# Kernel tuning notes

Hardware: AMD Instinct MI355X
Metric: run time of the kernel (lower is better)

The kernel has to match this reference:

```python
import jax, jax.numpy as jnp
import numpy as np

K = 2  # diffusion order
N, S, D, L, C = 4000, 32, 128, 2, 10
THETA = 0.5


def setup_inputs() -> dict:
    key = jax.random.key(0)
    ks = jax.random.split(key, 16)
    w = 0.05  # weight scale to keep tanh/exp in sane range
    return {
        "A": jax.random.uniform(ks[0], (N, N), dtype=jnp.float32),
        "embs": jax.random.normal(ks[1], (L, S, N, D), dtype=jnp.float32),
        "conv1_w": jax.random.normal(ks[2], (K, D, D), dtype=jnp.float32) * w,
        "conv2_w": jax.random.normal(ks[3], (K, D, D), dtype=jnp.float32) * w,
        "lin_in_w": jax.random.normal(ks[4], (D, D), dtype=jnp.float32) * w,
        "lin_out_w": jax.random.normal(ks[5], (D, 2 * D), dtype=jnp.float32) * w,
        "W_psi": jax.random.normal(ks[6], (2 * D, D), dtype=jnp.float32) * w,
        "b_psi": jax.random.normal(ks[7], (D,), dtype=jnp.float32) * w,
        "ae": jax.random.uniform(ks[8], (N, 1, 1), dtype=jnp.float32),
        "ab": jax.random.uniform(ks[9], (N, 1, 1), dtype=jnp.float32),
        "emb_table": jax.random.uniform(ks[10], (N, D), minval=-0.1, maxval=0.1, dtype=jnp.float32),
        "W_p": jax.random.normal(ks[11], (D, C), dtype=jnp.float32) * w,
        "W_c": jax.random.normal(ks[12], (D, D), dtype=jnp.float32) * w,
    }


def _diffusion(A_tilde, X, W):
    # A_tilde: [N,N] (sym-normalized); X: [N,S,D] (linear in X, so batching over S
    # is identical to the per-timestep loop); W: [K,D,D]
    P_f = A_tilde / A_tilde.sum(axis=1, keepdims=True)
    P_v = A_tilde.T / A_tilde.sum(axis=0, keepdims=True)
    Z = jnp.einsum('mn,nsd->msd', P_f, X) @ W[0]
    P_psi_f, P_psi_v = P_f, P_v
    for k in range(1, K):
        if k < K // 2:
            P_psi_f = P_psi_f @ P_f
            M = P_psi_f
        else:
            P_psi_v = P_psi_v @ P_v
            M = P_psi_v
        Z = Z + jnp.einsum('mn,nsd->msd', M, X) @ W[k]
    return Z


def _attention(context, lin_in_w, lin_out_w, ae, ab):
    # context: [N,S,D]; query is the last timestep, output_len == 1
    q = context[:, -1, :] @ lin_in_w.T                    # [N,D]
    scores = jnp.einsum('nd,nsd->ns', q, context)         # [N,S]
    attw = jax.nn.softmax(scores, axis=-1)                # [N,S]
    mix = attw[:, None, :] * context.transpose(0, 2, 1)   # [N,D,S]
    delta_t = jnp.arange(S - 1, -1, -1, dtype=context.dtype)  # flipped arange
    bt = jnp.exp(-ab * delta_t[None, None, :])            # [N,1,S]
    term2 = jax.nn.relu(ae * mix * bt)                    # [N,D,S]
    mix_sum = (term2 + mix).sum(axis=-1)                  # [N,D]
    combined = jnp.concatenate([mix_sum, q], axis=-1)     # [N,2D]
    return jnp.tanh(combined @ lin_out_w.T)               # [N,D]


def reference(A, embs, conv1_w, conv2_w, lin_in_w, lin_out_w, W_psi, b_psi,
              ae, ab, emb_table, W_p, W_c):
    n = A.shape[0]
    A_t = A + jnp.eye(n, dtype=A.dtype)
    d_inv_sqrt = A_t.sum(axis=1) ** -0.5
    A_tilde = d_inv_sqrt[:, None] * A_t * d_inv_sqrt[None, :]

    outs = []
    for l in range(L):
        X = embs[l].transpose(1, 0, 2)                    # [N,S,D]
        h = _diffusion(A_tilde, X, conv1_w)
        h = jax.nn.relu(h)
        h = _diffusion(A_tilde, h, conv2_w)               # [N,S,D]
        # fusion with theta = 0.5 (h_tilde is the raw embedding)
        fused = jnp.concatenate([THETA * h, (1.0 - THETA) * X], axis=-1) @ W_psi + b_psi
        outs.append(_attention(fused, lin_in_w, lin_out_w, ae, ab))
    outputs = jnp.stack(outs)                             # [L,N,D]

    # embedding lookup over arange(N) is an identity gather
    qs = jax.nn.relu(emb_table)                           # [N,D]
    betas = jnp.exp(jnp.einsum('nd,lne->lde', qs, jnp.tanh(outputs)))  # [L,D,D]
    betas = betas / betas.sum(axis=0)
    Z = jnp.einsum('lnd,lde->ne', outputs, betas)         # [N,D]

    P = jax.nn.softmax(Z @ W_p, axis=1)                   # [N,C]
    C_mat = P.T @ Z                                       # [C,D]
    eta = P.T @ A @ P                                     # [C,C] (vectorized eta_ij)
    C_prime = jax.nn.relu(eta @ (C_mat @ W_c.T))          # [C,D]
    return P @ C_prime                                    # [N,D]
```

## Files before the change

### kernel.cpp

```cpp
#include <hip/hip_runtime.h>
#include <hip/hip_bf16.h>


typedef __attribute__((ext_vector_type(8))) short short8;
typedef __attribute__((ext_vector_type(4))) float f32x4;
typedef __attribute__((ext_vector_type(4))) unsigned short us4;

__device__ __forceinline__ unsigned short f2bf(float x) {
  unsigned int u = __builtin_bit_cast(unsigned int, x);
  u += 0x7FFFu + ((u >> 16) & 1u);
  return (unsigned short)(u >> 16);
}
__device__ __forceinline__ float bf2f(unsigned short u) {
  unsigned int x = ((unsigned int)u) << 16;
  return __builtin_bit_cast(float, x);
}

__device__ __forceinline__ void gload16(const void* g, void* l) {
  __builtin_amdgcn_global_load_lds((const __attribute__((address_space(1))) void*)g,
                                   (__attribute__((address_space(3))) void*)l, 16, 0, 0);
}

__device__ __forceinline__ void barrier_() {
  __builtin_amdgcn_sched_barrier(0);
  asm volatile("" ::: "memory");
  __builtin_amdgcn_s_barrier();
  asm volatile("" ::: "memory");
  __builtin_amdgcn_sched_barrier(0);
}

template<int TRANS, int RELU>
__global__ __launch_bounds__(512, 2)
void gemm256(const unsigned short* __restrict__ Ap, int lda,
             const unsigned short* __restrict__ Bp, int ldb,
             unsigned short* __restrict__ outp, int ldo, int K)
{
  __shared__ alignas(16) unsigned short lds[81920];
  const int t = threadIdx.x;
  const int lane = t & 63;
  const int wave = t >> 6;
  const int wm = wave >> 2;
  const int wn = wave & 3;
  const int lrow = lane & 15;
  const int kgrp = lane >> 4;
  const int slotbase = (kgrp ^ (lrow & 7)) << 3;

  const int b = blockIdx.x;
  const int wg = (b & 7) * 32 + (b >> 3);
  const int m0 = (wg >> 4) << 8;
  const int j0 = (wg & 15) << 8;

  const int prow = t >> 3;
  const int lslot = (t & 7) ^ (prow & 7);
  const unsigned short* srcA = Ap + (size_t)(m0 + prow) * lda + lslot * 8;
  const unsigned short* srcB = Bp + (size_t)(j0 + prow) * ldb + lslot * 8;
  const size_t a64 = (size_t)64 * lda, a128 = (size_t)128 * lda;
  const size_t b64 = (size_t)64 * ldb, b128 = (size_t)128 * ldb;
  unsigned short* dA = &lds[t * 8];
  unsigned short* dB = &lds[32768 + t * 8];
  const int NT = K >> 6;

#define STG_A(h, kb, kt) { const unsigned short* s_ = srcA + (h)*a128 + (size_t)(kt)*64; \
    gload16(s_, dA + (kb)*16384 + (h)*8192); \
    gload16(s_ + a64, dA + (kb)*16384 + (h)*8192 + 4096); }
#define STG_B(h, bb, kt) { const unsigned short* s_ = srcB + (h)*b128 + (size_t)(kt)*64; \
    gload16(s_, dB + (bb)*16384 + (h)*8192); \
    gload16(s_ + b64, dB + (bb)*16384 + (h)*8192 + 4096); }

  const int arb = wm * 8192 + lrow * 64 + slotbase;
  const int brb = (wn >> 1) * 8192 + ((wn & 1) << 12) + lrow * 64 + slotbase;

#define RD_A(dst, base_off) \
  _Pragma("unroll") for (int mf_ = 0; mf_ < 4; ++mf_) { \
    dst[mf_][0] = *(const short8*)&lds[(base_off) + mf_*1024]; \
    dst[mf_][1] = *(const short8*)&lds[((base_off) ^ 32) + mf_*1024]; }
#define RD_B(dst, base_off) \
  _Pragma("unroll") for (int nf_ = 0; nf_ < 2; ++nf_) { \
    dst[nf_][0] = *(const short8*)&lds[(base_off) + nf_*1024]; \
    dst[nf_][1] = *(const short8*)&lds[((base_off) ^ 32) + nf_*1024]; }

#define MFMA16(AF, BF, MB, NB) \
  _Pragma("unroll") for (int mf_ = 0; mf_ < 4; ++mf_) \
  _Pragma("unroll") for (int nf_ = 0; nf_ < 2; ++nf_) { \
    acc[(MB)+mf_][(NB)+nf_] = __builtin_amdgcn_mfma_f32_16x16x32_bf16(AF[mf_][0], BF[nf_][0], acc[(MB)+mf_][(NB)+nf_], 0,0,0); \
    acc[(MB)+mf_][(NB)+nf_] = __builtin_amdgcn_mfma_f32_16x16x32_bf16(AF[mf_][1], BF[nf_][1], acc[(MB)+mf_][(NB)+nf_], 0,0,0); }

#define LGKM(n) { asm volatile("s_waitcnt lgkmcnt(" #n ")" ::: "memory"); \
                  __builtin_amdgcn_sched_barrier(0); }

  f32x4 acc[8][4];
#pragma unroll
  for (int i = 0; i < 8; ++i)
#pragma unroll
    for (int j = 0; j < 4; ++j) acc[i][j] = f32x4{0.f, 0.f, 0.f, 0.f};

  short8 a0[4][2], a1[4][2], b0[2][2], b1[2][2];

  STG_B(0, 0, 0); STG_B(1, 0, 0); STG_A(0, 0, 0); STG_A(1, 0, 0);
  STG_B(0, 1, 1); STG_B(1, 1, 1); STG_A(0, 1, 1); STG_A(1, 1, 1);
  asm volatile("s_waitcnt vmcnt(8)" ::: "memory");
  barrier_();
  RD_A(a0, arb);
  RD_B(b0, 32768 + brb);

  int rb3 = 0, rn3 = 1, sb3 = 2;
  for (int V = 0; V < NT; ++V) {
    const int abuf  = (V & 1) << 14;
    const int anbuf = ((V + 1) & 1) << 14;
    const int bbuf  = 32768 + (rb3 << 14);
    const int bnbuf = 32768 + (rn3 << 14);
    const bool stg = (V + 2 < NT);
    const bool rdn = (V + 1 < NT);

    RD_B(b1, bbuf + brb + 2048);
    LGKM(4);
    if (stg) STG_B(0, sb3, V + 2);
    __builtin_amdgcn_s_setprio(1);
    MFMA16(a0, b0, 0, 0);
    __builtin_amdgcn_s_setprio(0);
    barrier_();

    RD_A(a1, abuf + arb + 4096);
    LGKM(8);
    if (stg) STG_B(1, sb3, V + 2);
    __builtin_amdgcn_s_setprio(1);
    MFMA16(a0, b1, 0, 2);
    __builtin_amdgcn_s_setprio(0);
    if (stg) { asm volatile("s_waitcnt vmcnt(4)" ::: "memory"); }
    else     { asm volatile("s_waitcnt vmcnt(0)" ::: "memory"); }
    barrier_();

    if (rdn) { RD_A(a0, anbuf + arb); LGKM(8); }
    else     { LGKM(0); }
    if (stg) STG_A(0, (V & 1), V + 2);
    __builtin_amdgcn_s_setprio(1);
    MFMA16(a1, b0, 4, 0);
    __builtin_amdgcn_s_setprio(0);
    barrier_();

    if (rdn) { RD_B(b0, bnbuf + brb); LGKM(4); }
    else     { LGKM(0); }
    if (stg) STG_A(1, (V & 1), V + 2);
    __builtin_amdgcn_s_setprio(1);
    MFMA16(a1, b1, 4, 2);
    __builtin_amdgcn_s_setprio(0);
    barrier_();

    rb3 = rn3; rn3 = (rn3 == 2) ? 0 : rn3 + 1;
    sb3 = (sb3 == 2) ? 0 : sb3 + 1;
  }

  if (TRANS) {
#pragma unroll
    for (int mf = 0; mf < 8; ++mf) {
#pragma unroll
      for (int nf = 0; nf < 4; ++nf) {
        const int ml = wm * 128 + mf * 16 + kgrp * 4;
        const int jl = wn * 64 + nf * 16 + lrow;
        const int gm = ml >> 2;
        us4 pk;
#pragma unroll
        for (int r = 0; r < 4; ++r) pk[r] = f2bf(acc[mf][nf][r]);
        *(us4*)&lds[jl * 256 + ((gm ^ (jl & 7)) << 2)] = pk;
      }
    }
    barrier_();
#pragma unroll
    for (int i = 0; i < 32; ++i) {
      const int r = i * 8 + (t >> 6);
      const int c = t & 63;
      us4 v = *(const us4*)&lds[r * 256 + ((c ^ (r & 7)) << 2)];
      *(us4*)(outp + (size_t)(j0 + r) * ldo + m0 + c * 4) = v;
    }
  } else {
#pragma unroll
    for (int mf = 0; mf < 8; ++mf) {
#pragma unroll
      for (int nf = 0; nf < 4; ++nf) {
        const int m = m0 + wm * 128 + mf * 16 + kgrp * 4;
        const int j = j0 + wn * 64 + nf * 16 + lrow;
#pragma unroll
        for (int r = 0; r < 4; ++r) {
          float v = acc[mf][nf][r];
          if (RELU) v = fmaxf(v, 0.f);
          outp[(size_t)(m + r) * ldo + j] = f2bf(v);
        }
      }
    }
  }
#undef STG_A
#undef STG_B
#undef RD_A
#undef RD_B
#undef MFMA16
#undef LGKM
}

template<int EPI, int KFULL, int MINB, int Z32>
__global__ __launch_bounds__(256, MINB)
void gemm_smallk(const unsigned short* __restrict__ A1,
                 const unsigned short* __restrict__ A2,
                 int k_switch, int a_zstride, int lda,
                 const unsigned short* __restrict__ B, int ldb,
                 void* __restrict__ outp,
                 long o_j, long o_m, long o_z, long o_jt,
                 const float* __restrict__ bias,
                 const unsigned short* __restrict__ B2,
                 float* __restrict__ out2,
                 const float* __restrict__ bias2)
{
  __shared__ alignas(16) unsigned short At[(KFULL / 32) * 4096];
  __shared__ alignas(16) unsigned short Bt[(KFULL / 32) * 4096];
  const int t = threadIdx.x;
  const int lane = t & 63;
  const int wave = t >> 6;
  const int m0 = blockIdx.x << 7;
  const int jt = blockIdx.y;
  const int j0 = jt << 7;
  const int z  = blockIdx.z;
  const bool isq = Z32 && (z == 32);
  const int ze = isq ? 31 : z;
  const unsigned short* Bp = isq ? B2 : B;
  const int wm = (wave >> 1) << 6;
  const int wn = (wave & 1) << 6;
  const int lrow = lane & 15;
  const int kgrp = lane >> 4;

  const unsigned short* A1z = A1 + (long)ze * a_zstride;
  const unsigned short* A2z = A2 + (long)ze * a_zstride;

  const int r0 = t >> 2, q0 = t & 3;
  const int c1 = t + 256;
  const int r1 = c1 >> 2, q1 = c1 & 3;

#pragma unroll
  for (int kk = 0; kk < KFULL / 32; ++kk) {
    const int k0 = kk * 32;
    const unsigned short* As; int ka;
    if (k0 < k_switch) { As = A1z; ka = k0; } else { As = A2z; ka = k0 - k_switch; }
    gload16(As + (long)(m0 + r0) * lda + ka + q0 * 8, At + kk * 4096 + t * 8);
    gload16(As + (long)(m0 + r1) * lda + ka + q1 * 8, At + kk * 4096 + c1 * 8);
    gload16(Bp + (long)(j0 + r0) * ldb + k0 + q0 * 8, Bt + kk * 4096 + t * 8);
    gload16(Bp + (long)(j0 + r1) * ldb + k0 + q1 * 8, Bt + kk * 4096 + c1 * 8);
  }
  __syncthreads();

  f32x4 acc[4][4];
#pragma unroll
  for (int i = 0; i < 4; ++i)
#pragma unroll
    for (int j = 0; j < 4; ++j) acc[i][j] = f32x4{0.f, 0.f, 0.f, 0.f};

#pragma unroll
  for (int kk = 0; kk < KFULL / 32; ++kk) {
    short8 af[4], bv[4];
#pragma unroll
    for (int i = 0; i < 4; ++i)
      af[i] = *(const short8*)(At + kk * 4096 + (wm + i * 16 + lrow) * 32 + kgrp * 8);
#pragma unroll
    for (int i = 0; i < 4; ++i)
      bv[i] = *(const short8*)(Bt + kk * 4096 + (wn + i * 16 + lrow) * 32 + kgrp * 8);
#pragma unroll
    for (int i = 0; i < 4; ++i)
#pragma unroll
      for (int j = 0; j < 4; ++j)
        acc[i][j] = __builtin_amdgcn_mfma_f32_16x16x32_bf16(af[i], bv[j], acc[i][j], 0, 0, 0);
  }

  const int mlb = wm + kgrp * 4;
  if (EPI == 0) {
    __syncthreads();
#pragma unroll
    for (int i = 0; i < 4; ++i) {
#pragma unroll
      for (int j = 0; j < 4; ++j) {
        const int jl = wn + j * 16 + lrow;
        const int ml = mlb + i * 16;
        const int gm = ml >> 2;
        us4 pk;
#pragma unroll
        for (int r = 0; r < 4; ++r) pk[r] = f2bf(acc[i][j][r]);
        *(us4*)&At[jl * 128 + ((gm ^ (jl & 7)) << 2)] = pk;
      }
    }
    __syncthreads();
#pragma unroll
    for (int i = 0; i < 16; ++i) {
      const int r = i * 8 + (t >> 5);
      const int c = t & 31;
      us4 v = *(const us4*)&At[r * 128 + ((c ^ (r & 7)) << 2)];
      long base = (long)r * o_j + (long)(m0 + c * 4) * o_m + (long)z * o_z + (long)jt * o_jt;
      *(us4*)((unsigned short*)outp + base) = v;
    }
    return;
  }

#pragma unroll
  for (int i = 0; i < 4; ++i) {
#pragma unroll
    for (int j = 0; j < 4; ++j) {
      const int jl = wn + j * 16 + lrow;
      const int ml = mlb + i * 16;
      if (EPI == 2) {
        if (isq) {
          float badd = bias2[j0 + jl];
#pragma unroll
          for (int r = 0; r < 4; ++r)
            out2[(size_t)(m0 + ml + r) * 128 + (j0 + jl)] = acc[i][j][r] + badd;
        } else {
          float* of = (float*)outp;
          float badd = bias[j0 + jl];
#pragma unroll
          for (int r = 0; r < 4; ++r) {
            long idx = (long)jl * o_j + (long)(m0 + ml + r) * o_m + (long)z * o_z + (long)jt * o_jt;
            of[idx] = acc[i][j][r] + badd;
          }
        }
      } else {
        float* of = (float*)outp;
#pragma unroll
        for (int r = 0; r < 4; ++r) {
          int mm = m0 + ml + r;
          int n = mm & 4095, l = mm >> 12;
          if (n < 4000) {
            float o = tanhf(acc[i][j][r]);
            size_t idx = (size_t)l * 512000 + (size_t)n * 128 + (j0 + jl);
            of[idx] = o;
            out2[idx] = tanhf(o);
          }
        }
      }
    }
  }
}

__global__ __launch_bounds__(256) void rowsum_dis(const float* __restrict__ A,
                                                  float* __restrict__ dis) {
  int m = blockIdx.x;
  if (m >= 4000) { if (threadIdx.x == 0) dis[m] = 0.f; return; }
  const float* r = A + (long)m * 4000;
  float a = 0.f;
  for (int i = threadIdx.x; i < 1000; i += 256) {
    float4 v = ((const float4*)r)[i];
    a += v.x + v.y + v.z + v.w;
  }
  for (int o = 32; o; o >>= 1) a += __shfl_xor(a, o);
  __shared__ float ls[4];
  if ((threadIdx.x & 63) == 0) ls[threadIdx.x >> 6] = a;
  __syncthreads();
  if (threadIdx.x == 0) dis[m] = rsqrtf(1.f + ls[0] + ls[1] + ls[2] + ls[3]);
}

__global__ __launch_bounds__(256) void wrow_kernel(const float* __restrict__ A,
                                                   const float* __restrict__ dis,
                                                   float* __restrict__ iwrow) {
  int m = blockIdx.x;
  if (m >= 4000) { if (threadIdx.x == 0) iwrow[m] = 0.f; return; }
  const float* r = A + (long)m * 4000;
  float a = 0.f;
  for (int n = threadIdx.x; n < 4000; n += 256) a += r[n] * dis[n];
  for (int o = 32; o; o >>= 1) a += __shfl_xor(a, o);
  __shared__ float ls[4];
  if ((threadIdx.x & 63) == 0) ls[threadIdx.x >> 6] = a;
  __syncthreads();
  if (threadIdx.x == 0) iwrow[m] = 1.f / (ls[0] + ls[1] + ls[2] + ls[3] + dis[m]);
}

__global__ __launch_bounds__(256) void wcol_part(const float* __restrict__ A,
                                                 const float* __restrict__ dis,
                                                 float* __restrict__ part) {
  int j = blockIdx.x * 256 + threadIdx.x;
  int mz = blockIdx.y;
  float a = 0.f;
  if (j < 4000) {
    int ms = mz * 125;
    for (int m = ms; m < ms + 125; ++m) a += A[(long)m * 4000 + j] * dis[m];
  }
  part[(long)mz * 4096 + j] = a;
}

__global__ __launch_bounds__(256) void wcol_fin(const float* __restrict__ part,
                                                const float* __restrict__ dis,
                                                float* __restrict__ iwcol) {
  int j = blockIdx.x * 256 + threadIdx.x;
  float s = 0.f;
  for (int z = 0; z < 32; ++z) s += part[(long)z * 4096 + j];
  iwcol[j] = (j < 4000) ? 1.f / (s + dis[j]) : 0.f;
}

__global__ __launch_bounds__(256) void build_P(const float* __restrict__ A,
                                               const float* __restrict__ dis,
                                               const float* __restrict__ iwrow,
                                               const float* __restrict__ iwcol,
                                               unsigned short* __restrict__ Pcat,
                                               unsigned short* __restrict__ PV,
                                               unsigned short* __restrict__ PVT) {
  __shared__ float tile[64][65];
  int m0 = blockIdx.y * 64, n0 = blockIdx.x * 64;
#pragma unroll
  for (int i = 0; i < 16; ++i) {
    int idx = i * 256 + threadIdx.x;
    int lr = idx >> 6, lc = idx & 63;
    int m = m0 + lr, n = n0 + lc;
    float v = 0.f;
    if (m < 4000 && n < 4000) {
      float a = A[(long)m * 4000 + n];
      if (m == n) a += 1.f;
      v = a * dis[n];
    }
    Pcat[(long)m * 8192 + n] = f2bf(v * iwrow[m]);
    float pv = v * iwcol[m];
    PVT[(long)m * 4096 + n] = f2bf(pv);
    tile[lr][lc] = pv;
  }
  __syncthreads();
#pragma unroll
  for (int i = 0; i < 16; ++i) {
    int idx = i * 256 + threadIdx.x;
    int lr = idx >> 6, lc = idx & 63;
    PV[(long)(n0 + lr) * 4096 + (m0 + lc)] = f2bf(tile[lc][lr]);
  }
}

__global__ __launch_bounds__(256) void prep_weights(const float* __restrict__ lin_out,
                                                    const float* __restrict__ c1,
                                                    const float* __restrict__ c2,
                                                    const float* __restrict__ wpsi,
                                                    const float* __restrict__ embt,
                                                    unsigned short* __restrict__ CW1T,
                                                    unsigned short* __restrict__ CW2T,
                                                    unsigned short* __restrict__ WPST,
                                                    unsigned short* __restrict__ LWOB,
                                                    float* __restrict__ qs) {
  int i = blockIdx.x * 256 + threadIdx.x;
  if (i < 32768) {
    int j = i >> 7, kk = i & 127;
    CW1T[i] = f2bf(c1[(j >> 7) * 16384 + kk * 128 + (j & 127)]);
  } else if (i < 65536) {
    int k = i - 32768; int j = k >> 7, kk = k & 127;
    CW2T[k] = f2bf(c2[(j >> 7) * 16384 + kk * 128 + (j & 127)]);
  } else if (i < 98304) {
    int k = i - 65536; int e = k >> 8, d2 = k & 255;
    WPST[k] = f2bf(0.5f * wpsi[d2 * 128 + e]);
  } else if (i < 131072) {
    int k = i - 98304;
    LWOB[k] = f2bf(lin_out[k]);
  } else if (i < 643072) {
    int k = i - 131072;
    qs[k] = fmaxf(embt[k], 0.f);
  }
}

__global__ __launch_bounds__(256) void wq_prep(const float* __restrict__ lin_in,
                                               const float* __restrict__ bpsi,
                                               const unsigned short* __restrict__ WPST,
                                               unsigned short* __restrict__ WQ,
                                               float* __restrict__ BQ) {
  int b = blockIdx.x, t = threadIdx.x;
  if (b < 128) {
    int idx = b * 256 + t;
    int d = idx >> 8, k2 = idx & 255;
    float acc = 0.f;
    for (int e = 0; e < 128; ++e)
      acc += lin_in[d * 128 + e] * bf2f(WPST[e * 256 + k2]);
    WQ[idx] = f2bf(acc);
  } else if (t < 128) {
    float acc = 0.f;
    for (int e = 0; e < 128; ++e) acc += bpsi[e] * lin_in[t * 128 + e];
    BQ[t] = acc;
  }
}

__global__ __launch_bounds__(256) void convert_X(const float* __restrict__ embsL,
                                                 unsigned short* __restrict__ X) {
  long i4 = (long)blockIdx.x * 256 + threadIdx.x;
  long e = i4 << 2;
  int n = (int)(e >> 12);
  int r = (int)(e & 4095);
  us4 o;
  if (n < 4000) {
    int s = r >> 7, d = r & 127;
    float4 v = *(const float4*)(embsL + ((long)s * 4000 + n) * 128 + d);
    o[0] = f2bf(v.x); o[1] = f2bf(v.y); o[2] = f2bf(v.z); o[3] = f2bf(v.w);
  } else { o[0] = o[1] = o[2] = o[3] = 0; }
  *(us4*)(X + (long)n * 4096 + r) = o;
}

__global__ __launch_bounds__(128) void attention2(const float* __restrict__ F,
                                                  const float* __restrict__ Q,
                                                  const float* __restrict__ ae,
                                                  const float* __restrict__ ab,
                                                  unsigned short* __restrict__ CATl) {
  int n = blockIdx.x, t = threadIdx.x;
  if (n >= 4000) {
    CATl[(size_t)n * 256 + t] = 0;
    CATl[(size_t)n * 256 + 128 + t] = 0;
    return;
  }
  __shared__ float Fs[32 * 132];
  __shared__ float qv[128], attw[32], btv[32];
  const float* Fr = F + (long)n * 4096;
  for (int i = t; i < 4096; i += 128) { int s = i >> 7, d = i & 127; Fs[s * 132 + d] = Fr[i]; }
  qv[t] = Q[(long)n * 128 + t];
  __syncthreads();
  if (t < 32) {
    float sc = 0.f;
    for (int d = 0; d < 128; ++d) sc += qv[d] * Fs[t * 132 + d];
    float mx = sc;
    for (int o = 16; o; o >>= 1) mx = fmaxf(mx, __shfl_xor(mx, o, 32));
    float ex = expf(sc - mx), sm = ex;
    for (int o = 16; o; o >>= 1) sm += __shfl_xor(sm, o, 32);
    attw[t] = ex / sm;
  } else if (t >= 64 && t < 96) {
    int s = t - 64;
    btv[s] = expf(-ab[n] * (float)(31 - s));
  }
  __syncthreads();
  float aen = ae[n], acc = 0.f;
  for (int s = 0; s < 32; ++s) {
    float f = Fs[s * 132 + t];
    acc += attw[s] * (f + aen * btv[s] * fmaxf(f, 0.f));
  }
  CATl[(size_t)n * 256 + t] = f2bf(acc);
  CATl[(size_t)n * 256 + 128 + t] = f2bf(qv[t]);
}

__global__ __launch_bounds__(256) void betas_part(const float* __restrict__ qs,
                                                  const float* __restrict__ T,
                                                  float* __restrict__ out) {
  int e = threadIdx.x & 127, dl = threadIdx.x >> 7;
  int d = blockIdx.x * 2 + dl, l = blockIdx.y, nc = blockIdx.z;
  const float* Tl = T + (long)l * 512000;
  float acc = 0.f;
  int n0 = nc * 500;
  for (int n = n0; n < n0 + 500; ++n)
    acc += qs[(long)n * 128 + d] * Tl[(long)n * 128 + e];
  out[(long)nc * 32768 + (long)l * 16384 + d * 128 + e] = acc;
}

__global__ __launch_bounds__(256) void bnorm_kernel(const float* __restrict__ brawp,
                                                    float* __restrict__ bn) {
  int i = blockIdx.x * 256 + threadIdx.x;
  float s0 = 0.f, s1 = 0.f;
  for (int nc = 0; nc < 8; ++nc) {
    s0 += brawp[(long)nc * 32768 + i];
    s1 += brawp[(long)nc * 32768 + 16384 + i];
  }
  float b0 = expf(s0), b1 = expf(s1);
  float s = b0 + b1;
  bn[i] = b0 / s;
  bn[16384 + i] = b1 / s;
}

__global__ __launch_bounds__(256) void z_kernel(const float* __restrict__ outs,
                                                const float* __restrict__ bn,
                                                float* __restrict__ Zb) {
  int n = blockIdx.x * 2 + (threadIdx.x >> 7);
  int e = threadIdx.x & 127;
  float acc = 0.f;
  for (int l = 0; l < 2; ++l) {
    const float* orow = outs + ((long)l * 4000 + n) * 128;
    const float* brow = bn + (long)l * 16384;
    for (int d = 0; d < 128; ++d) acc += orow[d] * brow[d * 128 + e];
  }
  Zb[(long)n * 128 + e] = acc;
}

__global__ __launch_bounds__(256) void p_kernel(const float* __restrict__ Zb,
                                                const float* __restrict__ Wp,
                                                float* __restrict__ P) {
  int n = blockIdx.x * 4 + (threadIdx.x >> 6);
  int c = threadIdx.x & 63;
  float val = 0.f;
  if (c < 10) {
    const float* zr = Zb + (long)n * 128;
    for (int d = 0; d < 128; ++d) val += zr[d] * Wp[d * 10 + c];
  }
  float mx = val;
  for (int i = 0; i < 10; ++i) mx = fmaxf(mx, __shfl(val, i, 64));
  float ex = (c < 10) ? expf(val - mx) : 0.f;
  float sm = 0.f;
  for (int i = 0; i < 10; ++i) sm += __shfl(ex, i, 64);
  if (c < 12) P[(long)n * 12 + c] = (c < 10) ? ex / sm : 0.f;
}

__global__ __launch_bounds__(256) void ap_kernel(const float* __restrict__ A,
                                                 const float* __restrict__ P,
                                                 float* __restrict__ AP) {
  int m = blockIdx.x, t = threadIdx.x;
  const float* Ar = A + (long)m * 4000;
  float acc[10];
#pragma unroll
  for (int c = 0; c < 10; ++c) acc[c] = 0.f;
  for (int n = t; n < 4000; n += 256) {
    float a = Ar[n];
    const float* Pr = P + (long)n * 12;
#pragma unroll
    for (int c = 0; c < 10; ++c) acc[c] += a * Pr[c];
  }
#pragma unroll
  for (int c = 0; c < 10; ++c)
    for (int o = 32; o; o >>= 1) acc[c] += __shfl_xor(acc[c], o);
  __shared__ float ls[4][10];
  if ((t & 63) == 0)
    for (int c = 0; c < 10; ++c) ls[t >> 6][c] = acc[c];
  __syncthreads();
  if (t < 10) AP[(long)m * 12 + t] = ls[0][t] + ls[1][t] + ls[2][t] + ls[3][t];
  if (t >= 10 && t < 12) AP[(long)m * 12 + t] = 0.f;
}

__global__ __launch_bounds__(256) void etacm_part(const float* __restrict__ P,
                                                  const float* __restrict__ AP,
                                                  const float* __restrict__ Z,
                                                  float* __restrict__ peta,
                                                  float* __restrict__ pcm) {
  int b = blockIdx.x, t = threadIdx.x;
  int ms = b * 63, me = ms + 63; if (me > 4000) me = 4000;
  int i_ = t / 10, j_ = t % 10;
  float ea = 0.f;
  float ca[5];
#pragma unroll
  for (int k = 0; k < 5; ++k) ca[k] = 0.f;
  for (int m = ms; m < me; ++m) {
    if (t < 100) ea += P[(long)m * 12 + i_] * AP[(long)m * 12 + j_];
#pragma unroll
    for (int k = 0; k < 5; ++k) {
      int idx = t + 256 * k;
      int c = idx >> 7, e = idx & 127;
      ca[k] += P[(long)m * 12 + c] * Z[(long)m * 128 + e];
    }
  }
  if (t < 100) peta[(long)b * 100 + t] = ea;
#pragma unroll
  for (int k = 0; k < 5; ++k) pcm[(long)b * 1280 + t + 256 * k] = ca[k];
}

__global__ __launch_bounds__(256) void final_small(const float* __restrict__ peta,
                                                   const float* __restrict__ pcm,
                                                   const float* __restrict__ Wc,
                                                   float* __restrict__ cprime) {
  __shared__ float eta_s[100], cm_s[1280], tmp_s[1280];
  int t = threadIdx.x;
  if (t < 100) {
    float s = 0.f;
    for (int b = 0; b < 64; ++b) s += peta[(long)b * 100 + t];
    eta_s[t] = s;
  }
  for (int i = t; i < 1280; i += 256) {
    float s = 0.f;
    for (int b = 0; b < 64; ++b) s += pcm[(long)b * 1280 + i];
    cm_s[i] = s;
  }
  __syncthreads();
  for (int i = t; i < 1280; i += 256) {
    int c = i >> 7, d = i & 127;
    float s = 0.f;
    for (int e = 0; e < 128; ++e) s += cm_s[c * 128 + e] * Wc[d * 128 + e];
    tmp_s[i] = s;
  }
  __syncthreads();
  for (int i = t; i < 1280; i += 256) {
    int c = i >> 7, d = i & 127;
    float s = 0.f;
    for (int j = 0; j < 10; ++j) s += eta_s[c * 10 + j] * tmp_s[j * 128 + d];
    cprime[i] = fmaxf(s, 0.f);
  }
}

__global__ __launch_bounds__(256) void out_kernel(const float* __restrict__ P,
                                                  const float* __restrict__ cpr,
                                                  float* __restrict__ out) {
  int idx = blockIdx.x * 256 + threadIdx.x;
  int n = idx >> 7, d = idx & 127;
  float s = 0.f;
#pragma unroll
  for (int c = 0; c < 10; ++c) s += P[(long)n * 12 + c] * cpr[c * 128 + d];
  out[idx] = s;
}

extern "C" void kernel_launch(void* const* d_in, const int* in_sizes, int n_in,
                              void* d_out, int out_size, void* d_ws, size_t ws_size,
                              hipStream_t stream) {
  (void)in_sizes; (void)n_in; (void)out_size; (void)ws_size;
  const float* A      = (const float*)d_in[0];
  const float* embs   = (const float*)d_in[1];
  const float* conv1w = (const float*)d_in[2];
  const float* conv2w = (const float*)d_in[3];
  const float* lin_in = (const float*)d_in[4];
  const float* lin_out= (const float*)d_in[5];
  const float* Wpsi   = (const float*)d_in[6];
  const float* bpsi   = (const float*)d_in[7];
  const float* ae     = (const float*)d_in[8];
  const float* ab     = (const float*)d_in[9];
  const float* embt   = (const float*)d_in[10];
  const float* Wp     = (const float*)d_in[11];
  const float* Wc     = (const float*)d_in[12];
  float* out = (float*)d_out;
  char* ws = (char*)d_ws;

  size_t off = 0;
  auto alloc = [&](size_t b) { size_t r = off; off += (b + 255) & ~(size_t)255; return r; };
  unsigned short* PCAT = (unsigned short*)(ws + alloc((size_t)4096 * 8192 * 2));
  char*           BTF  = ws + alloc((size_t)4096 * 8192 * 2);
  unsigned short* BT   = (unsigned short*)BTF;
  float*          Ff   = (float*)BTF;
  unsigned short* XBF  = (unsigned short*)(ws + alloc((size_t)4096 * 4096 * 2));
  unsigned short* PV   = XBF;
  unsigned short* HBUF = (unsigned short*)(ws + alloc((size_t)4096 * 4096 * 2));
  unsigned short* PVT  = HBUF;
  float* DIS   = (float*)(ws + alloc(4096 * 4));
  float* IWROW = (float*)(ws + alloc(4096 * 4));
  float* IWCOL = (float*)(ws + alloc(4096 * 4));
  float* WCP   = (float*)(ws + alloc((size_t)32 * 4096 * 4));
  unsigned short* CW1T = (unsigned short*)(ws + alloc(32768 * 2));
  unsigned short* CW2T = (unsigned short*)(ws + alloc(32768 * 2));
  unsigned short* WPST = (unsigned short*)(ws + alloc(32768 * 2));
  unsigned short* LWOB = (unsigned short*)(ws + alloc(32768 * 2));
  unsigned short* WQ   = (unsigned short*)(ws + alloc(32768 * 2));
  float* BQ    = (float*)(ws + alloc(128 * 4));
  float* QBUF  = (float*)(ws + alloc((size_t)4096 * 128 * 4));
  unsigned short* CAT = (unsigned short*)(ws + alloc((size_t)8192 * 256 * 2));
  float* OUTS = (float*)(ws + alloc((size_t)2 * 4000 * 128 * 4));
  float* TT   = (float*)(ws + alloc((size_t)2 * 4000 * 128 * 4));
  float* QS   = (float*)(ws + alloc((size_t)4000 * 128 * 4));
  float* BRAWP= (float*)(ws + alloc((size_t)8 * 32768 * 4));
  float* BNRM = (float*)(ws + alloc(32768 * 4));
  float* ZB   = (float*)(ws + alloc((size_t)4000 * 128 * 4));
  float* PP   = (float*)(ws + alloc((size_t)4000 * 12 * 4));
  float* APB  = (float*)(ws + alloc((size_t)4000 * 12 * 4));
  float* PETA = (float*)(ws + alloc((size_t)64 * 100 * 4));
  float* PCM  = (float*)(ws + alloc((size_t)64 * 1280 * 4));
  float* CPR  = (float*)(ws + alloc(1280 * 4));

  const int BIG = 1 << 30;

  rowsum_dis<<<4096, 256, 0, stream>>>(A, DIS);
  wrow_kernel<<<4096, 256, 0, stream>>>(A, DIS, IWROW);
  wcol_part<<<dim3(16, 32), 256, 0, stream>>>(A, DIS, WCP);
  wcol_fin<<<16, 256, 0, stream>>>(WCP, DIS, IWCOL);
  prep_weights<<<2512, 256, 0, stream>>>(lin_out, conv1w, conv2w, Wpsi, embt,
                                         CW1T, CW2T, WPST, LWOB, QS);
  wq_prep<<<129, 256, 0, stream>>>(lin_in, bpsi, WPST, WQ, BQ);
  build_P<<<dim3(64, 64), 256, 0, stream>>>(A, DIS, IWROW, IWCOL, PCAT, PV, PVT);

  gemm256<1, 0><<<256, 512, 0, stream>>>(PVT, 4096, PV, 4096, PCAT + 4096, 8192, 4096);

  for (int l = 0; l < 2; ++l) {
    convert_X<<<16384, 256, 0, stream>>>(embs + (long)l * 32 * 4000 * 128, XBF);
    gemm_smallk<0, 128, 2, 0><<<dim3(32, 2, 32), 256, 0, stream>>>(
        XBF, XBF, BIG, 128, 4096, CW1T, 128,
        BT, 8192L, 1L, 128L * 8192, 4096L, nullptr, nullptr, nullptr, nullptr);
    gemm256<0, 1><<<256, 512, 0, stream>>>(PCAT, 8192, BT, 8192, HBUF, 4096, 8192);
    gemm_smallk<0, 128, 2, 0><<<dim3(32, 2, 32), 256, 0, stream>>>(
        HBUF, HBUF, BIG, 128, 4096, CW2T, 128,
        BT, 8192L, 1L, 128L * 8192, 4096L, nullptr, nullptr, nullptr, nullptr);
    gemm256<0, 0><<<256, 512, 0, stream>>>(PCAT, 8192, BT, 8192, HBUF, 4096, 8192);
    gemm_smallk<2, 256, 1, 1><<<dim3(32, 1, 33), 256, 0, stream>>>(
        HBUF, XBF, 128, 128, 4096, WPST, 256,
        Ff, 1L, 4096L, 128L, 0L, bpsi, WQ, QBUF, BQ);
    attention2<<<4096, 128, 0, stream>>>(Ff, QBUF, ae, ab, CAT + (size_t)l * 4096 * 256);
  }

  gemm_smallk<3, 256, 1, 0><<<dim3(64, 1, 1), 256, 0, stream>>>(
      CAT, CAT, BIG, 0, 256, LWOB, 256,
      OUTS, 0L, 0L, 0L, 0L, nullptr, nullptr, TT, nullptr);

  betas_part<<<dim3(64, 2, 8), 256, 0, stream>>>(QS, TT, BRAWP);
  bnorm_kernel<<<64, 256, 0, stream>>>(BRAWP, BNRM);
  z_kernel<<<2000, 256, 0, stream>>>(OUTS, BNRM, ZB);
  p_kernel<<<1000, 256, 0, stream>>>(ZB, Wp, PP);
  ap_kernel<<<4000, 256, 0, stream>>>(A, PP, APB);
  etacm_part<<<64, 256, 0, stream>>>(PP, APB, ZB, PETA, PCM);
  final_small<<<1, 256, 0, stream>>>(PETA, PCM, Wc, CPR);
  out_kernel<<<2000, 256, 0, stream>>>(PP, CPR, out);
}
```

Baseline: 1.469 ms.

## Store fused features as bf16, merge wq_prep into prep_weights, tile z_kernel

The fusion GEMM epilogue now writes its fused features in bf16 instead of fp32, and attention2 reads bf16 with vector loads, which halves that intermediate's traffic. wq_prep is folded into prep_weights and recomputes the bf16 W_psi values inline, saving one launch. z_kernel now stages the betas matrix in shared memory and computes eight rows per block instead of re-reading it from global memory. The bf16 features add rounding error to the attention inputs.

```diff
diff --git a/kernel.cpp b/kernel.cpp
--- a/kernel.cpp
+++ b/kernel.cpp
@@ -301,19 +301,19 @@
     for (int j = 0; j < 4; ++j) {
       const int jl = wn + j * 16 + lrow;
       const int ml = mlb + i * 16;
-      if (EPI == 2) {
+      if (EPI == 4) {
         if (isq) {
           float badd = bias2[j0 + jl];
 #pragma unroll
           for (int r = 0; r < 4; ++r)
             out2[(size_t)(m0 + ml + r) * 128 + (j0 + jl)] = acc[i][j][r] + badd;
         } else {
-          float* of = (float*)outp;
+          unsigned short* ob = (unsigned short*)outp;
           float badd = bias[j0 + jl];
 #pragma unroll
           for (int r = 0; r < 4; ++r) {
             long idx = (long)jl * o_j + (long)(m0 + ml + r) * o_m + (long)z * o_z + (long)jt * o_jt;
-            of[idx] = acc[i][j][r] + badd;
+            ob[idx] = f2bf(acc[i][j][r] + badd);
           }
         }
       } else {
@@ -427,11 +427,15 @@
                                                     const float* __restrict__ c2,
                                                     const float* __restrict__ wpsi,
                                                     const float* __restrict__ embt,
+                                                    const float* __restrict__ lin_in,
+                                                    const float* __restrict__ bpsi,
                                                     unsigned short* __restrict__ CW1T,
                                                     unsigned short* __restrict__ CW2T,
                                                     unsigned short* __restrict__ WPST,
                                                     unsigned short* __restrict__ LWOB,
-                                                    float* __restrict__ qs) {
+                                                    float* __restrict__ qs,
+                                                    unsigned short* __restrict__ WQ,
+                                                    float* __restrict__ BQ) {
   int i = blockIdx.x * 256 + threadIdx.x;
   if (i < 32768) {
     int j = i >> 7, kk = i & 127;
@@ -448,26 +452,18 @@
   } else if (i < 643072) {
     int k = i - 131072;
     qs[k] = fmaxf(embt[k], 0.f);
-  }
-}
-
-__global__ __launch_bounds__(256) void wq_prep(const float* __restrict__ lin_in,
-                                               const float* __restrict__ bpsi,
-                                               const unsigned short* __restrict__ WPST,
-                                               unsigned short* __restrict__ WQ,
-                                               float* __restrict__ BQ) {
-  int b = blockIdx.x, t = threadIdx.x;
-  if (b < 128) {
-    int idx = b * 256 + t;
-    int d = idx >> 8, k2 = idx & 255;
+  } else if (i < 675840) {
+    int k = i - 643072;
+    int d = k >> 8, k2 = k & 255;
     float acc = 0.f;
     for (int e = 0; e < 128; ++e)
-      acc += lin_in[d * 128 + e] * bf2f(WPST[e * 256 + k2]);
-    WQ[idx] = f2bf(acc);
-  } else if (t < 128) {
+      acc += lin_in[d * 128 + e] * bf2f(f2bf(0.5f * wpsi[k2 * 128 + e]));
+    WQ[k] = f2bf(acc);
+  } else if (i < 675968) {
+    int d = i - 675840;
     float acc = 0.f;
-    for (int e = 0; e < 128; ++e) acc += bpsi[e] * lin_in[t * 128 + e];
-    BQ[t] = acc;
+    for (int e = 0; e < 128; ++e) acc += bpsi[e] * lin_in[d * 128 + e];
+    BQ[d] = acc;
   }
 }
 
@@ -486,7 +482,7 @@
   *(us4*)(X + (long)n * 4096 + r) = o;
 }
 
-__global__ __launch_bounds__(128) void attention2(const float* __restrict__ F,
+__global__ __launch_bounds__(128) void attention2(const unsigned short* __restrict__ F,
                                                   const float* __restrict__ Q,
                                                   const float* __restrict__ ae,
                                                   const float* __restrict__ ab,
@@ -499,8 +495,14 @@
   }
   __shared__ float Fs[32 * 132];
   __shared__ float qv[128], attw[32], btv[32];
-  const float* Fr = F + (long)n * 4096;
-  for (int i = t; i < 4096; i += 128) { int s = i >> 7, d = i & 127; Fs[s * 132 + d] = Fr[i]; }
+  const unsigned short* Fr = F + (size_t)n * 4096;
+  for (int i = t; i < 1024; i += 128) {
+    us4 v = *(const us4*)(Fr + i * 4);
+    int base = i * 4;
+    int s = base >> 7, d = base & 127;
+    float* fp = &Fs[s * 132 + d];
+    fp[0] = bf2f(v[0]); fp[1] = bf2f(v[1]); fp[2] = bf2f(v[2]); fp[3] = bf2f(v[3]);
+  }
   qv[t] = Q[(long)n * 128 + t];
   __syncthreads();
   if (t < 32) {
@@ -555,15 +557,29 @@
 __global__ __launch_bounds__(256) void z_kernel(const float* __restrict__ outs,
                                                 const float* __restrict__ bn,
                                                 float* __restrict__ Zb) {
-  int n = blockIdx.x * 2 + (threadIdx.x >> 7);
-  int e = threadIdx.x & 127;
-  float acc = 0.f;
+  __shared__ float bns[16384];
+  int t = threadIdx.x, nb = blockIdx.x * 8;
+  float acc[4] = {0.f, 0.f, 0.f, 0.f};
   for (int l = 0; l < 2; ++l) {
-    const float* orow = outs + ((long)l * 4000 + n) * 128;
-    const float* brow = bn + (long)l * 16384;
-    for (int d = 0; d < 128; ++d) acc += orow[d] * brow[d * 128 + e];
-  }
-  Zb[(long)n * 128 + e] = acc;
+    __syncthreads();
+    for (int i = t; i < 16384; i += 256) bns[i] = bn[(size_t)l * 16384 + i];
+    __syncthreads();
+#pragma unroll
+    for (int k = 0; k < 4; ++k) {
+      int o = t + 256 * k;
+      int row = o >> 7, e = o & 127;
+      const float* orow = outs + ((size_t)l * 4000 + nb + row) * 128;
+      float a = acc[k];
+      for (int d = 0; d < 128; ++d) a += orow[d] * bns[d * 128 + e];
+      acc[k] = a;
+    }
+  }
+#pragma unroll
+  for (int k = 0; k < 4; ++k) {
+    int o = t + 256 * k;
+    int row = o >> 7, e = o & 127;
+    Zb[(size_t)(nb + row) * 128 + e] = acc[k];
+  }
 }
 
 __global__ __launch_bounds__(256) void p_kernel(const float* __restrict__ Zb,
@@ -703,7 +719,7 @@
   unsigned short* PCAT = (unsigned short*)(ws + alloc((size_t)4096 * 8192 * 2));
   char*           BTF  = ws + alloc((size_t)4096 * 8192 * 2);
   unsigned short* BT   = (unsigned short*)BTF;
-  float*          Ff   = (float*)BTF;
+  unsigned short* FB   = (unsigned short*)BTF;
   unsigned short* XBF  = (unsigned short*)(ws + alloc((size_t)4096 * 4096 * 2));
   unsigned short* PV   = XBF;
   unsigned short* HBUF = (unsigned short*)(ws + alloc((size_t)4096 * 4096 * 2));
@@ -738,9 +754,9 @@
   wrow_kernel<<<4096, 256, 0, stream>>>(A, DIS, IWROW);
   wcol_part<<<dim3(16, 32), 256, 0, stream>>>(A, DIS, WCP);
   wcol_fin<<<16, 256, 0, stream>>>(WCP, DIS, IWCOL);
-  prep_weights<<<2512, 256, 0, stream>>>(lin_out, conv1w, conv2w, Wpsi, embt,
-                                         CW1T, CW2T, WPST, LWOB, QS);
-  wq_prep<<<129, 256, 0, stream>>>(lin_in, bpsi, WPST, WQ, BQ);
+  prep_weights<<<2641, 256, 0, stream>>>(lin_out, conv1w, conv2w, Wpsi, embt,
+                                         lin_in, bpsi,
+                                         CW1T, CW2T, WPST, LWOB, QS, WQ, BQ);
   build_P<<<dim3(64, 64), 256, 0, stream>>>(A, DIS, IWROW, IWCOL, PCAT, PV, PVT);
 
   gemm256<1, 0><<<256, 512, 0, stream>>>(PVT, 4096, PV, 4096, PCAT + 4096, 8192, 4096);
@@ -755,10 +771,10 @@
         HBUF, HBUF, BIG, 128, 4096, CW2T, 128,
         BT, 8192L, 1L, 128L * 8192, 4096L, nullptr, nullptr, nullptr, nullptr);
     gemm256<0, 0><<<256, 512, 0, stream>>>(PCAT, 8192, BT, 8192, HBUF, 4096, 8192);
-    gemm_smallk<2, 256, 1, 1><<<dim3(32, 1, 33), 256, 0, stream>>>(
+    gemm_smallk<4, 256, 1, 1><<<dim3(32, 1, 33), 256, 0, stream>>>(
         HBUF, XBF, 128, 128, 4096, WPST, 256,
-        Ff, 1L, 4096L, 128L, 0L, bpsi, WQ, QBUF, BQ);
-    attention2<<<4096, 128, 0, stream>>>(Ff, QBUF, ae, ab, CAT + (size_t)l * 4096 * 256);
+        FB, 1L, 4096L, 128L, 0L, bpsi, WQ, QBUF, BQ);
+    attention2<<<4096, 128, 0, stream>>>(FB, QBUF, ae, ab, CAT + (size_t)l * 4096 * 256);
   }
 
   gemm_smallk<3, 256, 1, 0><<<dim3(64, 1, 1), 256, 0, stream>>>(
@@ -767,7 +783,7 @@
 
   betas_part<<<dim3(64, 2, 8), 256, 0, stream>>>(QS, TT, BRAWP);
   bnorm_kernel<<<64, 256, 0, stream>>>(BRAWP, BNRM);
-  z_kernel<<<2000, 256, 0, stream>>>(OUTS, BNRM, ZB);
+  z_kernel<<<500, 256, 0, stream>>>(OUTS, BNRM, ZB);
   p_kernel<<<1000, 256, 0, stream>>>(ZB, Wp, PP);
   ap_kernel<<<4000, 256, 0, stream>>>(A, PP, APB);
   etacm_part<<<64, 256, 0, stream>>>(PP, APB, ZB, PETA, PCM);
```

Result: no change. 1.480 ms (+0.8%).
